# Performance work log

Measured on AMD Instinct MI355X. Metric: run time of the kernel, lower is better.

The kernel has to match this reference:

```python
import jax, jax.numpy as jnp
import numpy as np

HIDDEN = 512

def setup_inputs() -> dict:
    key = jax.random.key(0)
    ks = jax.random.split(key, 8)
    S, Bsz, I, H, D = 512, 64, 512, HIDDEN, 2
    return {
        "X": jax.random.normal(ks[0], (S, Bsz, I), jnp.float32),
        "W": jax.random.normal(ks[1], (D, 4 * H, I), jnp.float32) * 0.05,
        "R": jax.random.normal(ks[2], (D, 4 * H, H), jnp.float32) * 0.05,
        "B": jax.random.normal(ks[3], (D, 8 * H), jnp.float32) * 0.05,
        "sequence_lens": jax.random.randint(ks[4], (Bsz,), 0, S, jnp.int32),
        "initial_h": jax.random.normal(ks[5], (D, Bsz, H), jnp.float32) * 0.1,
        "initial_c": jax.random.normal(ks[6], (D, Bsz, H), jnp.float32) * 0.1,
        "P": jax.random.normal(ks[7], (D, 3 * H), jnp.float32) * 0.05,
    }

def _run_dir(Xg, R_d, Rb_d, h0, c0, P_d, seq_lens, ts, H):
    # Gate layout along 4H axis: i, o, f, c (ONNX order used by the source).
    P_i, P_f, P_o = P_d[:H], P_d[H:2 * H], P_d[2 * H:3 * H]

    def step(carry, inp):
        h, c = carry
        xg, t = inp                              # xg: [B,4H] precomputed X@W^T + Wb
        g = xg + h @ R_d.T + Rb_d                # [B,4H]
        i_t = jax.nn.sigmoid(g[:, :H] + P_i * c)
        f_t = jax.nn.sigmoid(g[:, 2 * H:3 * H] + P_f * c)
        c_til = jnp.tanh(g[:, 3 * H:4 * H])
        c_new = f_t * c + i_t * c_til
        o_t = jax.nn.sigmoid(g[:, H:2 * H] + P_o * c_new)
        h_new = o_t * jnp.tanh(c_new)
        mask = (t < seq_lens).astype(h_new.dtype)[:, None]
        h_new = h_new * mask + h0 * (1 - mask)
        c_new = c_new * mask + c0 * (1 - mask)
        return (h_new, c_new), h_new

    (h_f, c_f), hs = jax.lax.scan(step, (h0, c0), (Xg[ts], jnp.asarray(ts)))
    return hs, h_f, c_f

def reference(X, W, R, B, sequence_lens, initial_h, initial_c, P):
    S, Bsz, I = X.shape
    D = W.shape[0]
    H = W.shape[1] // 4
    Wb = B[:, :4 * H]
    Rb = B[:, 4 * H:8 * H]
    # Batch the input projection over all timesteps once: [D,S,B,4H]
    Xg_all = jnp.einsum('sbi,dgi->dsbg', X, W) + Wb[:, None, None, :]
    Ys, Yhs, Ycs = [], [], []
    for d in range(D):
        ts = np.arange(S) if d == 0 else np.arange(S)[::-1].copy()
        hs, h_f, c_f = _run_dir(Xg_all[d], R[d], Rb[d], initial_h[d],
                                initial_c[d], P[d], sequence_lens, ts, H)
        if d == 1:
            hs = hs[::-1]                         # scan emitted reversed time order
        Ys.append(hs)
        Yhs.append(h_f)
        Ycs.append(c_f)
    Y = jnp.stack(Ys, axis=1)                     # [S, D, B, H]
    Y_h = jnp.stack(Yhs, axis=0)                  # [D, B, H]
    Y_c = jnp.stack(Ycs, axis=0)                  # [D, B, H]
    return Y, Y_h, Y_c
```

## Files before the change

kernel.cpp:

```cpp
#include <hip/hip_runtime.h>
#include <stdint.h>
#include <stddef.h>

#define S_LEN 512
#define BATCH 64
#define ISZ   512
#define HID   512
#define NDIR  2

typedef short bf16x8 __attribute__((ext_vector_type(8)));
typedef unsigned short u16x8 __attribute__((ext_vector_type(8)));
typedef float f32x4 __attribute__((ext_vector_type(4)));

#define XB_ELEMS  ((size_t)S_LEN * 4 * 8192)
#define HH_ELEMS  ((size_t)NDIR * 513 * 4 * 8192)
#define CNT_BYTES ((size_t)16416)
#define XB_BYTES  (XB_ELEMS * 2)
#define HH_BYTES  (HH_ELEMS * 2)

__device__ __forceinline__ unsigned short f2bf(float f) {
    unsigned int u = __float_as_uint(f);
    u += 0x7fffu + ((u >> 16) & 1u);
    return (unsigned short)(u >> 16);
}

__device__ __forceinline__ int poll1_l2(const int* p) {
    int v;
    asm volatile("global_load_dword %0, %1, off sc0\n\t"
                 "s_waitcnt vmcnt(0)"
                 : "=&v"(v) : "v"(p) : "memory");
    return v;
}
__device__ __forceinline__ int poll1_llc(const int* p) {
    int v;
    asm volatile("global_load_dword %0, %1, off sc0 sc1\n\t"
                 "s_waitcnt vmcnt(0)"
                 : "=&v"(v) : "v"(p) : "memory");
    return v;
}

__global__ void k_convX(const float* __restrict__ X, unsigned short* __restrict__ Xb) {
    int gu = blockIdx.x * 256 + threadIdx.x;
    int t   = gu >> 12;
    int rem = gu & 4095;
    int b   = rem >> 6;
    int u   = rem & 63;
    const float* src = X + ((size_t)(t * 64 + b)) * 512 + u * 8;
    float4 a = *(const float4*)(src);
    float4 c = *(const float4*)(src + 4);
    u16x8 o;
    o[0]=f2bf(a.x); o[1]=f2bf(a.y); o[2]=f2bf(a.z); o[3]=f2bf(a.w);
    o[4]=f2bf(c.x); o[5]=f2bf(c.y); o[6]=f2bf(c.z); o[7]=f2bf(c.w);
    int i = b >> 4, br = b & 15;
    size_t off = ((size_t)(t * 4 + i)) * 8192 + (size_t)br * 512 + (size_t)((u ^ (b & 7)) << 3);
    *(u16x8*)(Xb + off) = o;
}

__global__ void k_initH(const float* __restrict__ h0, unsigned short* __restrict__ hh) {
    int gu = blockIdx.x * 256 + threadIdx.x;
    int d   = gu >> 12;
    int rem = gu & 4095;
    int b   = rem >> 6;
    int u   = rem & 63;
    const float* src = h0 + ((size_t)(d * 64 + b)) * 512 + u * 8;
    float4 a = *(const float4*)(src);
    float4 c = *(const float4*)(src + 4);
    u16x8 o;
    o[0]=f2bf(a.x); o[1]=f2bf(a.y); o[2]=f2bf(a.z); o[3]=f2bf(a.w);
    o[4]=f2bf(c.x); o[5]=f2bf(c.y); o[6]=f2bf(c.z); o[7]=f2bf(c.w);
    int i = b >> 4, br = b & 15;
    size_t blk = ((size_t)d * 513 + 0) * 4 + i;
    size_t off = blk * 8192 + (size_t)br * 512 + (size_t)((u ^ (b & 7)) << 3);
    *(u16x8*)(hh + off) = o;
}

__launch_bounds__(256, 1)
__global__ void k_lstm(const float* __restrict__ W, const float* __restrict__ R,
                       const float* __restrict__ Bb, const int* __restrict__ slen,
                       const float* __restrict__ h0g, const float* __restrict__ c0g,
                       const float* __restrict__ P,
                       const unsigned short* __restrict__ Xb,
                       unsigned short* __restrict__ hh,
                       int* __restrict__ cnt,
                       float* __restrict__ Y) {
    __shared__ __align__(16) float gbuf[4 * 256];
    __shared__ __align__(4) unsigned short hexch[256];
    __shared__ int s_xcd[256];
    __shared__ unsigned char s_inv[256];
    __shared__ int s_role, s_fast;

    const int tid = threadIdx.x;
    const int bx  = blockIdx.x;

    int* const arrive = cnt;
    int* const xcdtab = cnt + 288;

    if (tid == 0) {
        int x;
        asm volatile("s_getreg_b32 %0, hwreg(HW_REG_XCC_ID)" : "=s"(x));
        x &= 0xf;
        __hip_atomic_store(&xcdtab[bx], x + 1, __ATOMIC_RELAXED, __HIP_MEMORY_SCOPE_AGENT);
        asm volatile("s_waitcnt vmcnt(0)" ::: "memory");
        __hip_atomic_fetch_add(arrive, 1, __ATOMIC_RELAXED, __HIP_MEMORY_SCOPE_AGENT);
        int iters = 0;
        while (__hip_atomic_load(arrive, __ATOMIC_RELAXED, __HIP_MEMORY_SCOPE_AGENT) < 256) {
            __builtin_amdgcn_s_sleep(1);
            if (++iters > 2000000) break;
        }
    }
    __syncthreads();
    s_xcd[tid] = __hip_atomic_load(&xcdtab[tid], __ATOMIC_RELAXED, __HIP_MEMORY_SCOPE_AGENT) - 1;
    __syncthreads();
    {
        const int myx = s_xcd[tid];
        int r = 0;
        for (int b = 0; b < 256; ++b) {
            const int xb = s_xcd[b];
            r += (int)((xb < myx) | ((xb == myx) & (b < tid)));
        }
        s_inv[r] = (unsigned char)(myx & 0xff);
        if (tid == bx) s_role = r;
    }
    __syncthreads();
    if (tid == 0) {
        const int g0 = s_role & ~31;
        int uni = 1;
        for (int q = 1; q < 32; ++q) uni &= (int)(s_inv[g0 + q] == s_inv[g0]);
        int distinct = 1;
        for (int q = 1; q < 256; ++q) distinct += (int)(s_inv[q] != s_inv[q - 1]);
        s_fast = uni & (int)(distinct >= 2);
    }
    __syncthreads();
    const int  role = s_role;
    const bool fast = (s_fast != 0);
    const int  d = role >> 7;
    const int  i = (role >> 5) & 3;
    const int  j = role & 31;
    int* const gflags = cnt + 576 + ((role >> 5) << 5);

    const int w  = tid >> 6;
    const int l  = tid & 63;
    const int lr = l & 15;
    const int lq = l >> 4;

    bf16x8 Wf[16], Rf[16];
    {
        const int row = w * 512 + j * 16 + lr;
        const float* wp = W + ((size_t)(d * 2048 + row)) * 512;
        const float* rp = R + ((size_t)(d * 2048 + row)) * 512;
#pragma unroll
        for (int kc = 0; kc < 16; ++kc) {
            int k0 = kc * 32 + lq * 8;
            float4 a = *(const float4*)(wp + k0);
            float4 b4 = *(const float4*)(wp + k0 + 4);
            bf16x8 f;
            f[0]=(short)f2bf(a.x);  f[1]=(short)f2bf(a.y);  f[2]=(short)f2bf(a.z);  f[3]=(short)f2bf(a.w);
            f[4]=(short)f2bf(b4.x); f[5]=(short)f2bf(b4.y); f[6]=(short)f2bf(b4.z); f[7]=(short)f2bf(b4.w);
            Wf[kc] = f;
            a  = *(const float4*)(rp + k0);
            b4 = *(const float4*)(rp + k0 + 4);
            bf16x8 g;
            g[0]=(short)f2bf(a.x);  g[1]=(short)f2bf(a.y);  g[2]=(short)f2bf(a.z);  g[3]=(short)f2bf(a.w);
            g[4]=(short)f2bf(b4.x); g[5]=(short)f2bf(b4.y); g[6]=(short)f2bf(b4.z); g[7]=(short)f2bf(b4.w);
            Rf[kc] = g;
        }
    }

    const int eb = tid >> 4;
    const int ec = tid & 15;
    const int bg = i * 16 + eb;
    const int kh = j * 16 + ec;
    const float bias_i = Bb[d * 4096 + 0 * 512 + kh] + Bb[d * 4096 + 2048 + 0 * 512 + kh];
    const float bias_o = Bb[d * 4096 + 1 * 512 + kh] + Bb[d * 4096 + 2048 + 1 * 512 + kh];
    const float bias_f = Bb[d * 4096 + 2 * 512 + kh] + Bb[d * 4096 + 2048 + 2 * 512 + kh];
    const float bias_c = Bb[d * 4096 + 3 * 512 + kh] + Bb[d * 4096 + 2048 + 3 * 512 + kh];
    const float Pi = P[d * 1536 + kh];
    const float Pf = P[d * 1536 + 512 + kh];
    const float Po = P[d * 1536 + 1024 + kh];
    const int   sl  = slen[bg];
    const float h0v = h0g[((size_t)d * 64 + bg) * 512 + kh];
    const float c0v = c0g[((size_t)d * 64 + bg) * 512 + kh];
    float c_state = c0v;

    const int rbase = lr * 512;
    const int swz   = lr & 7;

    const int peb = tid >> 3;
    const int pm  = tid & 7;
    const size_t puo = (size_t)peb * 256
                     + (size_t)((((2 * j + (pm >> 2)) ^ (peb & 7)) << 2) + (pm & 3));

    int* const myflag = gflags + j;
    const int* const pollp = gflags + (l & 31);

    for (int ts = 0; ts < 512; ++ts) {
        const int t = (d == 0) ? ts : (511 - ts);

        f32x4 acc = {0.f, 0.f, 0.f, 0.f};
        {
            const unsigned short* xsrc = Xb + ((size_t)(t * 4 + i)) * 8192;
#pragma unroll
            for (int kc = 0; kc < 16; ++kc) {
                int u = (kc * 4 + lq) ^ swz;
                bf16x8 a = *(const bf16x8*)(xsrc + rbase + u * 8);
                acc = __builtin_amdgcn_mfma_f32_16x16x32_bf16(a, Wf[kc], acc, 0, 0, 0);
            }
        }

        if (ts > 0) {
            if (w == 0) {
                int iters = 0;
                if (fast) {
                    for (;;) {
                        int v = poll1_l2(pollp);
                        if (__all(v >= ts)) break;
                        __builtin_amdgcn_s_sleep(1);
                        if (++iters > 4000000) break;
                    }
                } else {
                    for (;;) {
                        int v = poll1_llc(pollp);
                        if (__all(v >= ts)) break;
                        __builtin_amdgcn_s_sleep(1);
                        if (++iters > 4000000) break;
                    }
                }
            }
            __syncthreads();
        }

        {
            const unsigned short* hsrc16 = hh + (((size_t)d * 513 + ts) * 4 + i) * 8192;
            if (fast) {
                bf16x8 hf[16];
#pragma unroll
                for (int kc = 0; kc < 16; ++kc) {
                    const int u = (kc * 4 + lq) ^ swz;
                    hf[kc] = *(const bf16x8*)(hsrc16 + rbase + u * 8);
                }
#pragma unroll
                for (int kc = 0; kc < 16; ++kc)
                    acc = __builtin_amdgcn_mfma_f32_16x16x32_bf16(hf[kc], Rf[kc], acc, 0, 0, 0);
            } else {
                const unsigned int* hsrc = (const unsigned int*)hsrc16;
                unsigned int hv[64];
#pragma unroll
                for (int kc = 0; kc < 16; ++kc) {
                    int u = (kc * 4 + lq) ^ swz;
                    const unsigned int* p = hsrc + (lr * 256 + u * 4);
                    hv[kc * 4 + 0] = __hip_atomic_load(p + 0, __ATOMIC_RELAXED, __HIP_MEMORY_SCOPE_AGENT);
                    hv[kc * 4 + 1] = __hip_atomic_load(p + 1, __ATOMIC_RELAXED, __HIP_MEMORY_SCOPE_AGENT);
                    hv[kc * 4 + 2] = __hip_atomic_load(p + 2, __ATOMIC_RELAXED, __HIP_MEMORY_SCOPE_AGENT);
                    hv[kc * 4 + 3] = __hip_atomic_load(p + 3, __ATOMIC_RELAXED, __HIP_MEMORY_SCOPE_AGENT);
                }
#pragma unroll
                for (int kc = 0; kc < 16; ++kc) {
                    union { unsigned int u[4]; bf16x8 v; } cvt;
                    cvt.u[0] = hv[kc * 4 + 0];
                    cvt.u[1] = hv[kc * 4 + 1];
                    cvt.u[2] = hv[kc * 4 + 2];
                    cvt.u[3] = hv[kc * 4 + 3];
                    acc = __builtin_amdgcn_mfma_f32_16x16x32_bf16(cvt.v, Rf[kc], acc, 0, 0, 0);
                }
            }
        }

#pragma unroll
        for (int r = 0; r < 4; ++r) {
            int b = lq * 4 + r;
            gbuf[w * 256 + b * 16 + lr] = acc[r];
        }
        __syncthreads();

        float hn, cn;
        {
            float gi = gbuf[0 * 256 + tid] + bias_i;
            float go = gbuf[1 * 256 + tid] + bias_o;
            float gf = gbuf[2 * 256 + tid] + bias_f;
            float gc = gbuf[3 * 256 + tid] + bias_c;
            float c  = c_state;
            float it = 1.f / (1.f + __expf(-(gi + Pi * c)));
            float ft = 1.f / (1.f + __expf(-(gf + Pf * c)));
            float ct = 1.f - 2.f / (__expf(2.f * gc) + 1.f);
            cn = ft * c + it * ct;
            float ot = 1.f / (1.f + __expf(-(go + Po * cn)));
            hn = ot * (1.f - 2.f / (__expf(2.f * cn) + 1.f));
            if (t >= sl) { hn = h0v; cn = c0v; }
            c_state = cn;

            Y[(((size_t)t * 2 + d) * 64 + bg) * 512 + kh] = hn;
            if (ts == 511) {
                Y[(size_t)33554432 + ((size_t)d * 64 + bg) * 512 + kh] = hn;
                Y[(size_t)33619968 + ((size_t)d * 64 + bg) * 512 + kh] = cn;
            }
            hexch[tid] = f2bf(hn);
        }
        __syncthreads();

        if (tid < 128) {
            unsigned int v = ((const unsigned int*)hexch)[tid];
            unsigned int* hdst =
                (unsigned int*)(hh + (((size_t)d * 513 + (ts + 1)) * 4 + i) * 8192);
            if (fast) hdst[puo] = v;
            else __hip_atomic_store(hdst + puo, v, __ATOMIC_RELAXED,
                                    __HIP_MEMORY_SCOPE_AGENT);
        }
        asm volatile("s_waitcnt vmcnt(0)" ::: "memory");
        __syncthreads();
        if (tid == 0) {
            if (fast) __hip_atomic_store(myflag, ts + 1, __ATOMIC_RELAXED,
                                         __HIP_MEMORY_SCOPE_WORKGROUP);
            else      __hip_atomic_store(myflag, ts + 1, __ATOMIC_RELAXED,
                                         __HIP_MEMORY_SCOPE_AGENT);
        }
    }
}

extern "C" void kernel_launch(void* const* d_in, const int* in_sizes, int n_in,
                              void* d_out, int out_size, void* d_ws, size_t ws_size,
                              hipStream_t stream) {
    const float* X  = (const float*)d_in[0];
    const float* W  = (const float*)d_in[1];
    const float* R  = (const float*)d_in[2];
    const float* Bb = (const float*)d_in[3];
    const int*   sl = (const int*)d_in[4];
    const float* h0 = (const float*)d_in[5];
    const float* c0 = (const float*)d_in[6];
    const float* P  = (const float*)d_in[7];
    float* Y = (float*)d_out;

    unsigned short* Xb  = (unsigned short*)d_ws;
    unsigned short* hh  = (unsigned short*)((char*)d_ws + XB_BYTES);
    int*            cnt = (int*)((char*)d_ws + XB_BYTES + HH_BYTES);

    hipMemsetAsync(cnt, 0, CNT_BYTES, stream);

    k_convX<<<8192, 256, 0, stream>>>(X, Xb);
    k_initH<<<32, 256, 0, stream>>>(h0, hh);
    k_lstm<<<256, 256, 0, stream>>>(W, R, Bb, sl, h0, c0, P, Xb, hh, cnt, Y);
}
```

Before: 3.765 ms.

## Remap gates per wave to drop block barriers and use per-wave flags

Reassigns MFMA output rows so each wave computes all four gates for its own four hidden columns. The gate exchange then stays inside a wave's LDS slice, so all __syncthreads in the time loop are removed. Each wave now publishes its own h slice with its own flag, and every wave polls the group's 128 flags with dwordx2 loads. Two accumulators split the MFMA dependency chain, and Y stores are vectorised as float2 after a shuffle. The cost is four times as many flags and polls, and correctness now depends on wave-local LDS ordering with no barrier.

```diff
diff --git a/kernel.cpp b/kernel.cpp
--- a/kernel.cpp
+++ b/kernel.cpp
@@ -11,6 +11,7 @@
 typedef short bf16x8 __attribute__((ext_vector_type(8)));
 typedef unsigned short u16x8 __attribute__((ext_vector_type(8)));
 typedef float f32x4 __attribute__((ext_vector_type(4)));
+typedef int   i32x2 __attribute__((ext_vector_type(2)));
 
 #define XB_ELEMS  ((size_t)S_LEN * 4 * 8192)
 #define HH_ELEMS  ((size_t)NDIR * 513 * 4 * 8192)
@@ -24,16 +25,16 @@
     return (unsigned short)(u >> 16);
 }
 
-__device__ __forceinline__ int poll1_l2(const int* p) {
-    int v;
-    asm volatile("global_load_dword %0, %1, off sc0\n\t"
+__device__ __forceinline__ i32x2 poll2_l2(const int* p) {
+    i32x2 v;
+    asm volatile("global_load_dwordx2 %0, %1, off sc0\n\t"
                  "s_waitcnt vmcnt(0)"
                  : "=&v"(v) : "v"(p) : "memory");
     return v;
 }
-__device__ __forceinline__ int poll1_llc(const int* p) {
-    int v;
-    asm volatile("global_load_dword %0, %1, off sc0 sc1\n\t"
+__device__ __forceinline__ i32x2 poll2_llc(const int* p) {
+    i32x2 v;
+    asm volatile("global_load_dwordx2 %0, %1, off sc0 sc1\n\t"
                  "s_waitcnt vmcnt(0)"
                  : "=&v"(v) : "v"(p) : "memory");
     return v;
@@ -83,8 +84,7 @@
                        unsigned short* __restrict__ hh,
                        int* __restrict__ cnt,
                        float* __restrict__ Y) {
-    __shared__ __align__(16) float gbuf[4 * 256];
-    __shared__ __align__(4) unsigned short hexch[256];
+    __shared__ __align__(16) float xbuf[4 * 256];
     __shared__ int s_xcd[256];
     __shared__ unsigned char s_inv[256];
     __shared__ int s_role, s_fast;
@@ -136,21 +136,24 @@
     const int  d = role >> 7;
     const int  i = (role >> 5) & 3;
     const int  j = role & 31;
-    int* const gflags = cnt + 576 + ((role >> 5) << 5);
+    int* const gflags = cnt + 576 + ((role >> 5) << 7);
 
     const int w  = tid >> 6;
     const int l  = tid & 63;
-    const int lr = l & 15;
-    const int lq = l >> 4;
+    const int n  = l & 15;
+    const int q  = l >> 4;
+
+    const int gsel = n & 3;
+    const int csel = n >> 2;
 
     bf16x8 Wf[16], Rf[16];
     {
-        const int row = w * 512 + j * 16 + lr;
+        const int row = gsel * 512 + j * 16 + w * 4 + csel;
         const float* wp = W + ((size_t)(d * 2048 + row)) * 512;
         const float* rp = R + ((size_t)(d * 2048 + row)) * 512;
 #pragma unroll
         for (int kc = 0; kc < 16; ++kc) {
-            int k0 = kc * 32 + lq * 8;
+            int k0 = kc * 32 + q * 8;
             float4 a = *(const float4*)(wp + k0);
             float4 b4 = *(const float4*)(wp + k0 + 4);
             bf16x8 f;
@@ -166,10 +169,10 @@
         }
     }
 
-    const int eb = tid >> 4;
-    const int ec = tid & 15;
-    const int bg = i * 16 + eb;
-    const int kh = j * 16 + ec;
+    const int bloc = l & 15;
+    const int cloc = l >> 4;
+    const int bg = i * 16 + bloc;
+    const int kh = j * 16 + w * 4 + cloc;
     const float bias_i = Bb[d * 4096 + 0 * 512 + kh] + Bb[d * 4096 + 2048 + 0 * 512 + kh];
     const float bias_o = Bb[d * 4096 + 1 * 512 + kh] + Bb[d * 4096 + 2048 + 1 * 512 + kh];
     const float bias_f = Bb[d * 4096 + 2 * 512 + kh] + Bb[d * 4096 + 2048 + 2 * 512 + kh];
@@ -182,51 +185,52 @@
     const float c0v = c0g[((size_t)d * 64 + bg) * 512 + kh];
     float c_state = c0v;
 
-    const int rbase = lr * 512;
-    const int swz   = lr & 7;
-
-    const int peb = tid >> 3;
-    const int pm  = tid & 7;
-    const size_t puo = (size_t)peb * 256
-                     + (size_t)((((2 * j + (pm >> 2)) ^ (peb & 7)) << 2) + (pm & 3));
-
-    int* const myflag = gflags + j;
-    const int* const pollp = gflags + (l & 31);
+    const int rbase = n * 512;
+    const int swz   = n & 7;
+
+    const int wrb = w * 256 + csel * 64 + gsel * 16 + q * 4;
+    const int erb = w * 256 + cloc * 64 + bloc;
+
+    const int pm  = w * 2 + (cloc >> 1);
+    const size_t puo = (size_t)bloc * 256
+                     + (size_t)((((2 * j + (pm >> 2)) ^ (bloc & 7)) << 2) + (pm & 3));
+
+    int* const myflag = gflags + (j * 4 + w);
+    const int* const pollp = gflags + 2 * l;
 
     for (int ts = 0; ts < 512; ++ts) {
         const int t = (d == 0) ? ts : (511 - ts);
 
-        f32x4 acc = {0.f, 0.f, 0.f, 0.f};
+        f32x4 acc0 = {0.f, 0.f, 0.f, 0.f};
+        f32x4 acc1 = {0.f, 0.f, 0.f, 0.f};
         {
             const unsigned short* xsrc = Xb + ((size_t)(t * 4 + i)) * 8192;
 #pragma unroll
             for (int kc = 0; kc < 16; ++kc) {
-                int u = (kc * 4 + lq) ^ swz;
+                int u = (kc * 4 + q) ^ swz;
                 bf16x8 a = *(const bf16x8*)(xsrc + rbase + u * 8);
-                acc = __builtin_amdgcn_mfma_f32_16x16x32_bf16(a, Wf[kc], acc, 0, 0, 0);
+                if (kc & 1) acc1 = __builtin_amdgcn_mfma_f32_16x16x32_bf16(a, Wf[kc], acc1, 0, 0, 0);
+                else        acc0 = __builtin_amdgcn_mfma_f32_16x16x32_bf16(a, Wf[kc], acc0, 0, 0, 0);
             }
         }
 
         if (ts > 0) {
-            if (w == 0) {
-                int iters = 0;
-                if (fast) {
-                    for (;;) {
-                        int v = poll1_l2(pollp);
-                        if (__all(v >= ts)) break;
-                        __builtin_amdgcn_s_sleep(1);
-                        if (++iters > 4000000) break;
-                    }
-                } else {
-                    for (;;) {
-                        int v = poll1_llc(pollp);
-                        if (__all(v >= ts)) break;
-                        __builtin_amdgcn_s_sleep(1);
-                        if (++iters > 4000000) break;
-                    }
+            int iters = 0;
+            if (fast) {
+                for (;;) {
+                    i32x2 f = poll2_l2(pollp);
+                    if (__all((f.x >= ts) & (f.y >= ts))) break;
+                    __builtin_amdgcn_s_sleep(1);
+                    if (++iters > 4000000) break;
+                }
+            } else {
+                for (;;) {
+                    i32x2 f = poll2_llc(pollp);
+                    if (__all((f.x >= ts) & (f.y >= ts))) break;
+                    __builtin_amdgcn_s_sleep(1);
+                    if (++iters > 4000000) break;
                 }
             }
-            __syncthreads();
         }
 
         {
@@ -235,19 +239,21 @@
                 bf16x8 hf[16];
 #pragma unroll
                 for (int kc = 0; kc < 16; ++kc) {
-                    const int u = (kc * 4 + lq) ^ swz;
+                    const int u = (kc * 4 + q) ^ swz;
                     hf[kc] = *(const bf16x8*)(hsrc16 + rbase + u * 8);
                 }
 #pragma unroll
-                for (int kc = 0; kc < 16; ++kc)
-                    acc = __builtin_amdgcn_mfma_f32_16x16x32_bf16(hf[kc], Rf[kc], acc, 0, 0, 0);
+                for (int kc = 0; kc < 16; ++kc) {
+                    if (kc & 1) acc1 = __builtin_amdgcn_mfma_f32_16x16x32_bf16(hf[kc], Rf[kc], acc1, 0, 0, 0);
+                    else        acc0 = __builtin_amdgcn_mfma_f32_16x16x32_bf16(hf[kc], Rf[kc], acc0, 0, 0, 0);
+                }
             } else {
                 const unsigned int* hsrc = (const unsigned int*)hsrc16;
                 unsigned int hv[64];
 #pragma unroll
                 for (int kc = 0; kc < 16; ++kc) {
-                    int u = (kc * 4 + lq) ^ swz;
-                    const unsigned int* p = hsrc + (lr * 256 + u * 4);
+                    int u = (kc * 4 + q) ^ swz;
+                    const unsigned int* p = hsrc + (n * 256 + u * 4);
                     hv[kc * 4 + 0] = __hip_atomic_load(p + 0, __ATOMIC_RELAXED, __HIP_MEMORY_SCOPE_AGENT);
                     hv[kc * 4 + 1] = __hip_atomic_load(p + 1, __ATOMIC_RELAXED, __HIP_MEMORY_SCOPE_AGENT);
                     hv[kc * 4 + 2] = __hip_atomic_load(p + 2, __ATOMIC_RELAXED, __HIP_MEMORY_SCOPE_AGENT);
@@ -260,24 +266,27 @@
                     cvt.u[1] = hv[kc * 4 + 1];
                     cvt.u[2] = hv[kc * 4 + 2];
                     cvt.u[3] = hv[kc * 4 + 3];
-                    acc = __builtin_amdgcn_mfma_f32_16x16x32_bf16(cvt.v, Rf[kc], acc, 0, 0, 0);
+                    if (kc & 1) acc1 = __builtin_amdgcn_mfma_f32_16x16x32_bf16(cvt.v, Rf[kc], acc1, 0, 0, 0);
+                    else        acc0 = __builtin_amdgcn_mfma_f32_16x16x32_bf16(cvt.v, Rf[kc], acc0, 0, 0, 0);
                 }
             }
         }
 
-#pragma unroll
-        for (int r = 0; r < 4; ++r) {
-            int b = lq * 4 + r;
-            gbuf[w * 256 + b * 16 + lr] = acc[r];
-        }
-        __syncthreads();
+        {
+            f32x4 accs = acc0 + acc1;
+            *(f32x4*)&xbuf[wrb] = accs;
+        }
+        const float g0 = xbuf[erb];
+        const float g1 = xbuf[erb + 16];
+        const float g2 = xbuf[erb + 32];
+        const float g3 = xbuf[erb + 48];
 
         float hn, cn;
         {
-            float gi = gbuf[0 * 256 + tid] + bias_i;
-            float go = gbuf[1 * 256 + tid] + bias_o;
-            float gf = gbuf[2 * 256 + tid] + bias_f;
-            float gc = gbuf[3 * 256 + tid] + bias_c;
+            float gi = g0 + bias_i;
+            float go = g1 + bias_o;
+            float gf = g2 + bias_f;
+            float gc = g3 + bias_c;
             float c  = c_state;
             float it = 1.f / (1.f + __expf(-(gi + Pi * c)));
             float ft = 1.f / (1.f + __expf(-(gf + Pf * c)));
@@ -287,18 +296,12 @@
             hn = ot * (1.f - 2.f / (__expf(2.f * cn) + 1.f));
             if (t >= sl) { hn = h0v; cn = c0v; }
             c_state = cn;
-
-            Y[(((size_t)t * 2 + d) * 64 + bg) * 512 + kh] = hn;
-            if (ts == 511) {
-                Y[(size_t)33554432 + ((size_t)d * 64 + bg) * 512 + kh] = hn;
-                Y[(size_t)33619968 + ((size_t)d * 64 + bg) * 512 + kh] = cn;
-            }
-            hexch[tid] = f2bf(hn);
-        }
-        __syncthreads();
-
-        if (tid < 128) {
-            unsigned int v = ((const unsigned int*)hexch)[tid];
+        }
+
+        const float hoth = __shfl_xor(hn, 16);
+        if ((l & 16) == 0) {
+            const unsigned int v = (unsigned int)f2bf(hn)
+                                 | ((unsigned int)f2bf(hoth) << 16);
             unsigned int* hdst =
                 (unsigned int*)(hh + (((size_t)d * 513 + (ts + 1)) * 4 + i) * 8192);
             if (fast) hdst[puo] = v;
@@ -306,12 +309,25 @@
                                     __HIP_MEMORY_SCOPE_AGENT);
         }
         asm volatile("s_waitcnt vmcnt(0)" ::: "memory");
-        __syncthreads();
-        if (tid == 0) {
+        if (l == 0) {
             if (fast) __hip_atomic_store(myflag, ts + 1, __ATOMIC_RELAXED,
                                          __HIP_MEMORY_SCOPE_WORKGROUP);
             else      __hip_atomic_store(myflag, ts + 1, __ATOMIC_RELAXED,
                                          __HIP_MEMORY_SCOPE_AGENT);
+        }
+
+        if ((l & 16) == 0) {
+            float2 yv; yv.x = hn; yv.y = hoth;
+            *(float2*)(Y + (((size_t)t * 2 + d) * 64 + bg) * 512 + kh) = yv;
+        }
+        if (ts == 511) {
+            const float coth = __shfl_xor(cn, 16);
+            if ((l & 16) == 0) {
+                float2 yh; yh.x = hn; yh.y = hoth;
+                float2 yc; yc.x = cn; yc.y = coth;
+                *(float2*)(Y + (size_t)33554432 + ((size_t)d * 64 + bg) * 512 + kh) = yh;
+                *(float2*)(Y + (size_t)33619968 + ((size_t)d * 64 + bg) * 512 + kh) = yc;
+            }
         }
     }
 }
```

Result: no change. 3.722 ms (-1.2%).
